# Kernel tuning notes

Measured on AMD Instinct MI355X. Metric: run time of the kernel, lower is better.

## Reference

```python
import jax, jax.numpy as jnp
import numpy as np

N, E, G, F, H, L, NH, HD = 40000, 640000, 256, 9, 128, 3, 4, 32
EPS = 1e-5

def _ln(x, g, b):
    m = jnp.mean(x, axis=-1, keepdims=True)
    v = jnp.mean((x - m) ** 2, axis=-1, keepdims=True)
    return (x - m) * jax.lax.rsqrt(v + EPS) * g + b

def _forward(floats, edge_index, batch):
    (x, pos, emb_w, emb_b, edge_w1, edge_b1, edge_w2, edge_b2,
     node_w1, node_b1, node_w2, node_b2, qkv_w, qkv_b, out_w, out_b,
     ln1_g, ln1_b, ln2_g, ln2_b, ff_w1, ff_b1, ff_w2, ff_b2,
     cls_w1, cls_b1, cls_w2, cls_b2) = floats
    src, dst = edge_index[0], edge_index[1]  # PyG: x_j = x[src], x_i = x[dst], aggregate at dst
    dist = jnp.linalg.norm(pos[dst] - pos[src], axis=-1, keepdims=True)  # [E,1]
    h = x @ emb_w + emb_b  # [N,H]
    for l in range(L):
        # message: edge_mlp(cat[x_i, x_j, dist])
        ef = jnp.concatenate([h[dst], h[src], dist], axis=-1)  # [E,2H+1]
        m = jax.nn.silu(ef @ edge_w1[l] + edge_b1[l])
        m = jax.nn.silu(m @ edge_w2[l] + edge_b2[l])  # [E,H]
        aggr = jax.ops.segment_sum(m, dst, num_segments=N)  # [N,H]
        u = jax.nn.silu(jnp.concatenate([h, aggr], axis=-1) @ node_w1[l] + node_b1[l])
        u = u @ node_w2[l] + node_b2[l]
        h = h + u  # residual in GAHT.forward
    # per-graph mean pooling (faithful to masked-mean loop)
    sums = jax.ops.segment_sum(h, batch, num_segments=G)  # [G,H]
    cnts = jax.ops.segment_sum(jnp.ones((N,), h.dtype), batch, num_segments=G)
    g = sums / jnp.maximum(cnts, 1.0)[:, None]  # [G,H]
    # 2-layer post-norm transformer encoder (batch=1, seq=G), relu FFN, eval mode (no dropout)
    scale = 1.0 / jnp.sqrt(jnp.asarray(HD, g.dtype))
    for t in range(2):
        qkv = g @ qkv_w[t] + qkv_b[t]  # [G,3H]
        q, k, v = jnp.split(qkv, 3, axis=-1)
        q = q.reshape(G, NH, HD); k = k.reshape(G, NH, HD); v = v.reshape(G, NH, HD)
        att = jax.nn.softmax(jnp.einsum('qhd,khd->hqk', q, k) * scale, axis=-1)
        o = jnp.einsum('hqk,khd->qhd', att, v).reshape(G, H)
        o = o @ out_w[t] + out_b[t]
        g = _ln(g + o, ln1_g[t], ln1_b[t])
        ff = jax.nn.relu(g @ ff_w1[t] + ff_b1[t]) @ ff_w2[t] + ff_b2[t]
        g = _ln(g + ff, ln2_g[t], ln2_b[t])
    out = jax.nn.relu(g @ cls_w1 + cls_b1) @ cls_w2 + cls_b2  # [G,1]
    return out.squeeze(-1)  # [G]


def setup_inputs() -> dict:
    key = jax.random.key(0)
    ks = jax.random.split(key, 16)
    def p(k, shape, scale=0.08):
        return jax.random.normal(k, shape, dtype=jnp.float32) * scale
    return {
        'x': jax.random.normal(ks[0], (N, F), dtype=jnp.float32),
        'pos': jax.random.normal(ks[1], (N, 3), dtype=jnp.float32),
        'emb_w': p(ks[2], (F, H)), 'emb_b': jnp.zeros((H,), jnp.float32),
        'edge_w1': p(ks[3], (L, 2 * H + 1, H)), 'edge_b1': jnp.zeros((L, H), jnp.float32),
        'edge_w2': p(ks[4], (L, H, H)), 'edge_b2': jnp.zeros((L, H), jnp.float32),
        'node_w1': p(ks[5], (L, 2 * H, H)), 'node_b1': jnp.zeros((L, H), jnp.float32),
        'node_w2': p(ks[6], (L, H, H)), 'node_b2': jnp.zeros((L, H), jnp.float32),
        'qkv_w': p(ks[7], (2, H, 3 * H)), 'qkv_b': jnp.zeros((2, 3 * H), jnp.float32),
        'out_w': p(ks[8], (2, H, H)), 'out_b': jnp.zeros((2, H), jnp.float32),
        'ln1_g': jnp.ones((2, H), jnp.float32), 'ln1_b': jnp.zeros((2, H), jnp.float32),
        'ln2_g': jnp.ones((2, H), jnp.float32), 'ln2_b': jnp.zeros((2, H), jnp.float32),
        'ff_w1': p(ks[9], (2, H, 2 * H)), 'ff_b1': jnp.zeros((2, 2 * H), jnp.float32),
        'ff_w2': p(ks[10], (2, 2 * H, H)), 'ff_b2': jnp.zeros((2, H), jnp.float32),
        'cls_w1': p(ks[11], (H, H // 2)), 'cls_b1': jnp.zeros((H // 2,), jnp.float32),
        'cls_w2': p(ks[12], (H // 2, 1)), 'cls_b2': jnp.zeros((1,), jnp.float32),
        'edge_index': jax.random.randint(ks[13], (2, E), 0, N),
        'batch': jnp.sort(jax.random.randint(ks[14], (N,), 0, G)),
    }


def reference(x, pos, emb_w, emb_b, edge_w1, edge_b1, edge_w2, edge_b2,
              node_w1, node_b1, node_w2, node_b2, qkv_w, qkv_b, out_w, out_b,
              ln1_g, ln1_b, ln2_g, ln2_b, ff_w1, ff_b1, ff_w2, ff_b2,
              cls_w1, cls_b1, cls_w2, cls_b2, edge_index, batch):
    floats = (x, pos, emb_w, emb_b, edge_w1, edge_b1, edge_w2, edge_b2,
              node_w1, node_b1, node_w2, node_b2, qkv_w, qkv_b, out_w, out_b,
              ln1_g, ln1_b, ln2_g, ln2_b, ff_w1, ff_b1, ff_w2, ff_b2,
              cls_w1, cls_b1, cls_w2, cls_b2)
    return _forward(floats, edge_index, batch)
```

## Files before the change

kernel.cpp:

```cpp
#include <hip/hip_runtime.h>
#include <hip/hip_bf16.h>
#include <stdint.h>

#define NN 40000
#define EE 640000
#define GG 256
#define FFE 9
#define HH 128

typedef __bf16 bf16;
typedef __bf16 bf16x8 __attribute__((ext_vector_type(8)));
typedef float f32x4 __attribute__((ext_vector_type(4)));

__device__ __forceinline__ f32x4 mfma16(bf16x8 a, bf16x8 b, f32x4 c){
  return __builtin_amdgcn_mfma_f32_16x16x32_bf16(a, b, c, 0, 0, 0);
}
__device__ __forceinline__ float silu_f(float x){
  return x * __builtin_amdgcn_rcpf(1.0f + __expf(-x));
}
__device__ __forceinline__ uint16_t bfb(float x){ bf16 h=(bf16)x; return *(uint16_t*)&h; }
__device__ __forceinline__ int swz(int row, int cb){
  return row*256 + (cb ^ ((row & 7) << 4));
}

__global__ __launch_bounds__(256) void k_prep(
    const float* __restrict__ edge_w1, const float* __restrict__ edge_w2,
    const float* __restrict__ node_w1, const float* __restrict__ node_w2,
    const float* __restrict__ edge_b1,
    const float* __restrict__ x, const float* __restrict__ emb_w,
    const float* __restrict__ emb_b,
    bf16* __restrict__ wcatT, bf16* __restrict__ w2T,
    bf16* __restrict__ nw1T, bf16* __restrict__ nw2T,
    float* __restrict__ bcat, float* __restrict__ h,
    int* __restrict__ cnt)
{
  int b = blockIdx.x, tid = threadIdx.x;
  if (b < 192){
    int l = b/64; int t2 = (b%64)*256 + tid;
    int n = t2 >> 7, k = t2 & 127;
    wcatT[(size_t)l*32768 + n*128 + k] = (bf16)edge_w1[(size_t)l*32896 + k*128 + n];
  } else if (b < 384){
    int lb = b - 192; int l = lb/64; int t2 = (lb%64)*256 + tid;
    int n = t2 >> 7, k = t2 & 127;
    wcatT[(size_t)l*32768 + 16384 + n*128 + k] = (bf16)edge_w1[(size_t)l*32896 + (128+k)*128 + n];
  } else if (b < 576){
    int lb = b - 384; int l = lb/64; int t2 = (lb%64)*256 + tid;
    int n = t2 >> 7, k = t2 & 127;
    w2T[(size_t)l*16384 + n*128 + k] = (bf16)edge_w2[(size_t)l*16384 + k*128 + n];
  } else if (b < 960){
    int lb = b - 576; int l = lb/128; int t2 = (lb%128)*256 + tid;
    int n = t2 >> 8, k = t2 & 255;
    nw1T[(size_t)l*32768 + n*256 + k] = (bf16)node_w1[(size_t)l*32768 + k*128 + n];
  } else if (b < 1152){
    int lb = b - 960; int l = lb/64; int t2 = (lb%64)*256 + tid;
    int n = t2 >> 7, k = t2 & 127;
    nw2T[(size_t)l*16384 + n*128 + k] = (bf16)node_w2[(size_t)l*16384 + k*128 + n];
  } else if (b < 1155){
    int l = b - 1152;
    bcat[l*256 + tid] = (tid < 128) ? edge_b1[l*128 + tid] : 0.0f;
  } else if (b < 1312){
    int i = (b - 1155)*256 + tid;
    if (i < NN) cnt[i] = 0;
  } else {
    int idx = (b - 1312)*256 + tid;
    int n = idx >> 7, f = idx & 127;
    float s = emb_b[f];
    const float* xr = x + n*FFE;
    #pragma unroll
    for (int k=0;k<FFE;++k) s += xr[k]*emb_w[k*HH + f];
    h[idx] = s;
  }
}

__global__ __launch_bounds__(256) void k_hist(const int* __restrict__ dst, int* __restrict__ cnt){
  int e = blockIdx.x*256 + threadIdx.x;
  if (e < EE) atomicAdd(&cnt[dst[e]], 1);
}

__global__ __launch_bounds__(1024) void k_scanA(const int* __restrict__ cnt,
    int* __restrict__ cursor, int* __restrict__ partials, int n)
{
  __shared__ int s_wsum[16];
  int tid = threadIdx.x, lane = tid & 63, wv = tid >> 6;
  int i = blockIdx.x*4096 + tid*4;
  int c0 = (i  <n)? cnt[i  ] : 0;
  int c1 = (i+1<n)? cnt[i+1] : 0;
  int c2 = (i+2<n)? cnt[i+2] : 0;
  int c3 = (i+3<n)? cnt[i+3] : 0;
  int t0 = c0, t1 = t0+c1, t2 = t1+c2, t3 = t2+c3;
  int xx = t3;
  #pragma unroll
  for (int off=1; off<64; off<<=1){ int t = __shfl_up(xx, off); if (lane>=off) xx += t; }
  if (lane==63) s_wsum[wv] = xx;
  __syncthreads();
  if (wv==0 && lane<16){
    int y = s_wsum[lane];
    #pragma unroll
    for (int off=1; off<16; off<<=1){ int t = __shfl_up(y, off, 16); if (lane>=off) y += t; }
    s_wsum[lane] = y;
  }
  __syncthreads();
  int woff = wv ? s_wsum[wv-1] : 0;
  int eb = woff + xx - t3;
  if (i  <n) cursor[i  ] = eb;
  if (i+1<n) cursor[i+1] = eb + t0;
  if (i+2<n) cursor[i+2] = eb + t1;
  if (i+3<n) cursor[i+3] = eb + t2;
  if (tid==1023) partials[blockIdx.x] = woff + xx;
}

__global__ __launch_bounds__(64) void k_scanB(int* __restrict__ partials, int nb){
  int lane = threadIdx.x;
  int v = (lane < nb) ? partials[lane] : 0;
  int x = v;
  #pragma unroll
  for (int off=1; off<64; off<<=1){ int t = __shfl_up(x, off); if (lane>=off) x += t; }
  if (lane < nb) partials[lane] = x - v;
}

__global__ __launch_bounds__(256) void k_scatter(
    const int* __restrict__ ei, const float* __restrict__ pos,
    int* __restrict__ cursor, const int* __restrict__ offs, int4* __restrict__ rec)
{
  int e = blockIdx.x*256 + threadIdx.x;
  if (e >= EE) return;
  int s = ei[e], d = ei[EE + e];
  int p = atomicAdd(&cursor[d], 1) + offs[d >> 12];
  float dx = pos[d*3+0]-pos[s*3+0];
  float dy = pos[d*3+1]-pos[s*3+1];
  float dz = pos[d*3+2]-pos[s*3+2];
  int4 rc; rc.x = s; rc.y = d; rc.z = __float_as_int(sqrtf(dx*dx+dy*dy+dz*dz)); rc.w = 0;
  rec[p] = rc;
}

__global__ __launch_bounds__(256) void k_pgen(
    const float* __restrict__ h, const bf16* __restrict__ wct,
    const float* __restrict__ bcv, bf16* __restrict__ P, float* __restrict__ aggr)
{
  __shared__ bf16 SA[64][136];
  __shared__ bf16 SW[128][136];
  int tid = threadIdx.x, lane = tid & 63, w = tid >> 6;
  int rsel = lane & 15, hi = lane >> 4;
  int m0 = blockIdx.x * 64;
  f32x4 z = {0.f,0.f,0.f,0.f};
  #pragma unroll
  for (int it=0; it<8; ++it)
    *(f32x4*)(aggr + (size_t)m0*128 + (size_t)(tid + it*256)*4) = z;
  #pragma unroll
  for (int it=0; it<4; ++it){
    int idx = tid + it*256;
    int row = idx >> 4, cg = (idx & 15)*8;
    const float* sp = h + (size_t)(m0+row)*128 + cg;
    f32x4 u0 = *(const f32x4*)sp, u1v = *(const f32x4*)(sp+4);
    bf16x8 vv;
    vv[0]=(bf16)u0[0]; vv[1]=(bf16)u0[1]; vv[2]=(bf16)u0[2]; vv[3]=(bf16)u0[3];
    vv[4]=(bf16)u1v[0]; vv[5]=(bf16)u1v[1]; vv[6]=(bf16)u1v[2]; vv[7]=(bf16)u1v[3];
    *(bf16x8*)&SA[row][cg] = vv;
  }
  __syncthreads();
  int urow = w*16 + rsel;
  for (int nh=0; nh<2; ++nh){
    #pragma unroll
    for (int it=0; it<8; ++it){
      int idx = tid + it*256;
      int row = idx >> 4, cg = (idx & 15)*8;
      *(bf16x8*)&SW[row][cg] = *(const bf16x8*)(wct + (size_t)(nh*128+row)*128 + cg);
    }
    __syncthreads();
    f32x4 acc[8];
    #pragma unroll
    for (int nt=0;nt<8;++nt)
      #pragma unroll
      for (int r=0;r<4;++r) acc[nt][r]=0.f;
    #pragma unroll
    for (int ks=0; ks<4; ++ks){
      int kb = ks*32 + hi*8;
      bf16x8 fa = *(const bf16x8*)&SA[urow][kb];
      #pragma unroll
      for (int nt=0;nt<8;++nt){
        bf16x8 fw = *(const bf16x8*)&SW[nt*16 + rsel][kb];
        acc[nt] = mfma16(fw, fa, acc[nt]);
      }
    }
    __syncthreads();
    #pragma unroll
    for (int nt=0;nt<8;++nt){
      int nb = nh*128 + nt*16 + 4*hi;
      f32x4 b4 = *(const f32x4*)(bcv + nb);
      uint2 pk;
      pk.x = (unsigned)bfb(acc[nt][0] + b4[0]) | ((unsigned)bfb(acc[nt][1] + b4[1]) << 16);
      pk.y = (unsigned)bfb(acc[nt][2] + b4[2]) | ((unsigned)bfb(acc[nt][3] + b4[3]) << 16);
      *(uint2*)(P + (size_t)(m0+urow)*256 + nb) = pk;
    }
  }
}

template<bool DOP>
__global__ __launch_bounds__(256) void k_node(
    float* h, float* aggr,
    const bf16* __restrict__ nw1t,
    const bf16* __restrict__ nw2t,
    const bf16* __restrict__ wct,
    const float* __restrict__ nb1, const float* __restrict__ nb2,
    const float* __restrict__ bcv,
    bf16* __restrict__ P)
{
  __shared__ bf16 SA[64][132];
  __shared__ bf16 SW[128][72];
  __shared__ bf16 SU[64][132];
  int tid = threadIdx.x, lane = tid & 63, w = tid >> 6;
  int rsel = lane & 15, hi = lane >> 4;
  int m0 = blockIdx.x * 64;
  int urow = w*16 + rsel;
  int grow = m0 + urow;

  f32x4 acc[8];
  #pragma unroll
  for (int nt=0;nt<8;++nt)
    #pragma unroll
    for (int r=0;r<4;++r) acc[nt][r]=0.f;

  for (int kq=0; kq<4; ++kq){
    const float* src = (kq < 2) ? (h + (size_t)m0*128 + kq*64)
                                : (aggr + (size_t)m0*128 + (kq-2)*64);
    #pragma unroll
    for (int it=0; it<2; ++it){
      int g = tid + it*256;
      int row = g >> 3, cg = (g & 7)*8;
      const float* sp = src + (size_t)row*128 + cg;
      f32x4 u0 = *(const f32x4*)sp, u1v = *(const f32x4*)(sp+4);
      bf16x8 vv;
      vv[0]=(bf16)u0[0]; vv[1]=(bf16)u0[1]; vv[2]=(bf16)u0[2]; vv[3]=(bf16)u0[3];
      vv[4]=(bf16)u1v[0]; vv[5]=(bf16)u1v[1]; vv[6]=(bf16)u1v[2]; vv[7]=(bf16)u1v[3];
      *(bf16x8*)&SA[row][cg] = vv;
    }
    #pragma unroll
    for (int it=0; it<4; ++it){
      int g = tid + it*256;
      int row = g >> 3, cg = (g & 7)*8;
      *(bf16x8*)&SW[row][cg] = *(const bf16x8*)(nw1t + (size_t)row*256 + kq*64 + cg);
    }
    __syncthreads();
    #pragma unroll
    for (int ks=0; ks<2; ++ks){
      int kb = ks*32 + hi*8;
      bf16x8 fa = *(const bf16x8*)&SA[w*16 + rsel][kb];
      #pragma unroll
      for (int nt=0;nt<8;++nt){
        bf16x8 fw = *(const bf16x8*)&SW[nt*16 + rsel][kb];
        acc[nt] = mfma16(fw, fa, acc[nt]);
      }
    }
    __syncthreads();
  }

  #pragma unroll
  for (int nt=0;nt<8;++nt){
    int nb = nt*16 + 4*hi;
    f32x4 b4 = *(const f32x4*)(nb1 + nb);
    uint2 pk;
    pk.x = (unsigned)bfb(silu_f(acc[nt][0] + b4[0])) | ((unsigned)bfb(silu_f(acc[nt][1] + b4[1])) << 16);
    pk.y = (unsigned)bfb(silu_f(acc[nt][2] + b4[2])) | ((unsigned)bfb(silu_f(acc[nt][3] + b4[3])) << 16);
    *(uint2*)&SU[urow][nb] = pk;
  }
  __syncthreads();

  #pragma unroll
  for (int nt=0;nt<8;++nt)
    #pragma unroll
    for (int r=0;r<4;++r) acc[nt][r]=0.f;
  for (int kq=0; kq<2; ++kq){
    #pragma unroll
    for (int it=0; it<4; ++it){
      int g = tid + it*256;
      int row = g >> 3, cg = (g & 7)*8;
      *(bf16x8*)&SW[row][cg] = *(const bf16x8*)(nw2t + (size_t)row*128 + kq*64 + cg);
    }
    __syncthreads();
    #pragma unroll
    for (int ks=0; ks<2; ++ks){
      int kb = ks*32 + hi*8;
      bf16x8 fa = *(const bf16x8*)&SU[w*16 + rsel][kq*64 + kb];
      #pragma unroll
      for (int nt=0;nt<8;++nt){
        bf16x8 fw = *(const bf16x8*)&SW[nt*16 + rsel][kb];
        acc[nt] = mfma16(fw, fa, acc[nt]);
      }
    }
    __syncthreads();
  }

  #pragma unroll
  for (int nt=0;nt<8;++nt){
    int nb = nt*16 + 4*hi;
    f32x4 b4 = *(const f32x4*)(nb2 + nb);
    f32x4 h4 = *(const f32x4*)(h + (size_t)grow*128 + nb);
    f32x4 v;
    #pragma unroll
    for (int r=0;r<4;++r) v[r] = h4[r] + acc[nt][r] + b4[r];
    *(f32x4*)(h + (size_t)grow*128 + nb) = v;
    uint2 pk;
    pk.x = (unsigned)bfb(v[0]) | ((unsigned)bfb(v[1]) << 16);
    pk.y = (unsigned)bfb(v[2]) | ((unsigned)bfb(v[3]) << 16);
    *(uint2*)&SA[urow][nb] = pk;
  }
  __syncthreads();

  if (DOP){
    for (int nh=0; nh<2; ++nh){
      #pragma unroll
      for (int nt=0;nt<8;++nt)
        #pragma unroll
        for (int r=0;r<4;++r) acc[nt][r]=0.f;
      for (int kq=0; kq<2; ++kq){
        #pragma unroll
        for (int it=0; it<4; ++it){
          int g = tid + it*256;
          int row = g >> 3, cg = (g & 7)*8;
          *(bf16x8*)&SW[row][cg] = *(const bf16x8*)(wct + (size_t)(nh*128+row)*128 + kq*64 + cg);
        }
        __syncthreads();
        #pragma unroll
        for (int ks=0; ks<2; ++ks){
          int kb = ks*32 + hi*8;
          bf16x8 fa = *(const bf16x8*)&SA[w*16 + rsel][kq*64 + kb];
          #pragma unroll
          for (int nt=0;nt<8;++nt){
            bf16x8 fw = *(const bf16x8*)&SW[nt*16 + rsel][kb];
            acc[nt] = mfma16(fw, fa, acc[nt]);
          }
        }
        __syncthreads();
      }
      #pragma unroll
      for (int nt=0;nt<8;++nt){
        int nb = nh*128 + nt*16 + 4*hi;
        f32x4 b4 = *(const f32x4*)(bcv + nb);
        uint2 pk;
        pk.x = (unsigned)bfb(acc[nt][0] + b4[0]) | ((unsigned)bfb(acc[nt][1] + b4[1]) << 16);
        pk.y = (unsigned)bfb(acc[nt][2] + b4[2]) | ((unsigned)bfb(acc[nt][3] + b4[3]) << 16);
        *(uint2*)(P + (size_t)grow*256 + nb) = pk;
      }
    }
    f32x4 z = {0.f,0.f,0.f,0.f};
    #pragma unroll
    for (int it=0; it<8; ++it){
      int idx = tid + it*256;
      *(f32x4*)(aggr + (size_t)m0*128 + (size_t)idx*4) = z;
    }
  }
}

__global__ __launch_bounds__(512, 6) void k_edge(
    const bf16* __restrict__ P, const bf16* __restrict__ w2t,
    const float* __restrict__ w1r, const float* __restrict__ b2,
    const int4* __restrict__ rec, float* __restrict__ aggr)
{
  __shared__ char smem[32768];
  __shared__ int s_dst[128];
  __shared__ int s_segid[128];
  __shared__ int s_segdst[128];
  __shared__ bf16 s_sel[16][136];
  __shared__ int s_misc[4];
  int tid = threadIdx.x, lane = tid & 63, w = tid >> 6;
  int rsel = lane & 15, hi = lane >> 4;
  int bid = blockIdx.x;
  int swb = (bid & 7) * (EE/128/8) + (bid >> 3);
  int e0 = swb * 128;
  int col = w*16 + rsel;

  bf16x8 fb[4];
  #pragma unroll
  for (int ks=0;ks<4;++ks)
    fb[ks] = *(const bf16x8*)(w2t + (size_t)col*128 + ks*32 + hi*8);

  if (tid == 0){
    s_misc[0] = (e0 == 0) ? -2147483647 : rec[e0-1].y;
    s_misc[1] = (e0 + 128 >= EE) ? -2147483647 : rec[e0+128].y;
  }

  int cq = (tid & 15)*8;
  int er = tid >> 4;
  int4 rc[4];
  #pragma unroll
  for (int it=0; it<4; ++it) rc[it] = rec[e0 + er + it*32];
  uint4 pau[4], pbu[4];
  #pragma unroll
  for (int it=0; it<4; ++it){
    pau[it] = *(const uint4*)(P + ((size_t)rc[it].y << 8) + cq);
    pbu[it] = *(const uint4*)(P + ((size_t)rc[it].x << 8) + 128 + cq);
  }
  if (cq == 0){
    #pragma unroll
    for (int it=0; it<4; ++it) s_dst[er + it*32] = rc[it].y;
  }
  f32x4 wr0 = *(const f32x4*)(w1r + cq);
  f32x4 wr1 = *(const f32x4*)(w1r + cq + 4);
  #pragma unroll
  for (int it=0; it<4; ++it){
    float dist = __int_as_float(rc[it].z);
    bf16x8 mm;
    #pragma unroll
    for (int j=0;j<4;++j){
      unsigned ua = ((const unsigned*)&pau[it])[j];
      unsigned ub = ((const unsigned*)&pbu[it])[j];
      float al = __uint_as_float(ua << 16);
      float ah = __uint_as_float(ua & 0xFFFF0000u);
      float bl = __uint_as_float(ub << 16);
      float bh = __uint_as_float(ub & 0xFFFF0000u);
      float wlo = (j<2) ? wr0[2*j]   : wr1[2*(j-2)];
      float whi = (j<2) ? wr0[2*j+1] : wr1[2*(j-2)+1];
      mm[2*j]   = (bf16)silu_f(al + bl + dist*wlo);
      mm[2*j+1] = (bf16)silu_f(ah + bh + dist*whi);
    }
    *(bf16x8*)(smem + swz(er + it*32, cq*2)) = mm;
  }
  __syncthreads();

  if (w == 0){
    int d0 = s_dst[2*lane], d1 = s_dst[2*lane+1];
    int dm1 = (lane == 0) ? 0 : s_dst[2*lane-1];
    int h0 = (lane == 0) ? 1 : (d0 != dm1);
    int h1 = (d1 != d0);
    int p = h0 + h1, x = p;
    #pragma unroll
    for (int off=1; off<64; off<<=1){ int t = __shfl_up(x, off); if (lane>=off) x += t; }
    int excl = x - p;
    int id0 = excl + h0 - 1;
    int id1 = excl + p - 1;
    s_segid[2*lane]   = id0;
    s_segid[2*lane+1] = id1;
    if (h0) s_segdst[id0] = d0;
    if (h1) s_segdst[id1] = d1;
    if (lane == 63) s_misc[2] = id1 + 1;
  }

  f32x4 acc[8];
  #pragma unroll
  for (int mt=0;mt<8;++mt)
    #pragma unroll
    for (int r=0;r<4;++r) acc[mt][r]=0.f;
  #pragma unroll
  for (int mt=0;mt<8;++mt){
    #pragma unroll
    for (int ks=0;ks<4;++ks){
      bf16x8 fa = *(const bf16x8*)(smem + swz(mt*16 + rsel, ks*64 + hi*16));
      acc[mt] = mfma16(fa, fb[ks], acc[mt]);
    }
  }
  __syncthreads();

  float bb = b2[col];
  #pragma unroll
  for (int mt=0;mt<8;++mt){
    uint2 pk;
    pk.x = (unsigned)bfb(silu_f(acc[mt][0] + bb)) | ((unsigned)bfb(silu_f(acc[mt][1] + bb)) << 16);
    pk.y = (unsigned)bfb(silu_f(acc[mt][2] + bb)) | ((unsigned)bfb(silu_f(acc[mt][3] + bb)) << 16);
    *(uint2*)(smem + col*256 + ((mt*32 + hi*8) ^ ((col & 7) << 4))) = pk;
  }
  __syncthreads();

  bf16x8 gb[4];
  #pragma unroll
  for (int ks=0;ks<4;++ks)
    gb[ks] = *(const bf16x8*)(smem + col*256 + ((ks*64 + hi*16) ^ ((col & 7) << 4)));
  int nseg = s_misc[2];
  bool openL = (s_dst[0]   == s_misc[0]);
  bool openR = (s_dst[127] == s_misc[1]);
  const bf16 ONE = (bf16)1.0f, ZERO = (bf16)0.0f;
  for (int st = 0; st < nseg; st += 16){
    __syncthreads();
    #pragma unroll
    for (int k4=0;k4<4;++k4){
      int idx = tid + k4*512;
      int s = idx >> 7, e = idx & 127;
      s_sel[s][e] = (s_segid[e] == st + s) ? ONE : ZERO;
    }
    __syncthreads();
    f32x4 racc = {0.f,0.f,0.f,0.f};
    #pragma unroll
    for (int ks=0;ks<4;++ks){
      bf16x8 sa = *(const bf16x8*)&s_sel[rsel][ks*32 + hi*8];
      racc = mfma16(sa, gb[ks], racc);
    }
    #pragma unroll
    for (int r=0;r<4;++r){
      int s = st + 4*hi + r;
      if (s < nseg){
        float v = racc[r];
        size_t off = (size_t)s_segdst[s]*128 + col;
        bool atom = (s == 0 && openL) || (s == nseg-1 && openR);
        if (atom) atomicAdd(&aggr[off], v);
        else      aggr[off] = v;
      }
    }
  }
}

__device__ __forceinline__ int lbound(const int* a, int n, int key){
  int lo=0, hi=n;
  while (lo<hi){ int mid=(lo+hi)>>1; if (a[mid]<key) lo=mid+1; else hi=mid; }
  return lo;
}

__global__ __launch_bounds__(384) void k_pool_qkv(
    const float* __restrict__ h, const int* __restrict__ batch,
    const float* __restrict__ wq, const float* __restrict__ bq,
    float* __restrict__ gbuf, float* __restrict__ qkvb)
{
  __shared__ float sg[128];
  int gr = blockIdx.x, tid = threadIdx.x;
  if (tid < 128){
    int lo = lbound(batch, NN, gr), hi2 = lbound(batch, NN, gr+1);
    float s = 0.f;
    for (int n=lo;n<hi2;++n) s += h[(size_t)n*HH + tid];
    int c = hi2 - lo; if (c < 1) c = 1;
    s /= (float)c;
    sg[tid] = s; gbuf[gr*128 + tid] = s;
  }
  __syncthreads();
  float a = bq[tid];
  for (int k=0;k<128;++k) a += sg[k]*wq[k*384 + tid];
  qkvb[gr*384 + tid] = a;
}

template<int MODE>
__global__ __launch_bounds__(128) void k_tail(
    const float* __restrict__ qkv, const float* __restrict__ wo,
    const float* __restrict__ bo, const float* __restrict__ l1g,
    const float* __restrict__ l1b, const float* __restrict__ w1,
    const float* __restrict__ b1f, const float* __restrict__ w2,
    const float* __restrict__ b2f, const float* __restrict__ l2g,
    const float* __restrict__ l2b, float* __restrict__ gbuf,
    const float* __restrict__ wq2, const float* __restrict__ bq2,
    float* __restrict__ qkvb2,
    const float* __restrict__ cw1, const float* __restrict__ cb1,
    const float* __restrict__ cw2, const float* __restrict__ cb2,
    float* __restrict__ out)
{
  __shared__ float sq[128];
  __shared__ float ss[4][256];
  __shared__ float so[128];
  __shared__ float st[256];
  __shared__ float red[4];
  int r = blockIdx.x, tid = threadIdx.x;
  sq[tid] = qkv[r*384 + tid];
  __syncthreads();
  const float scale = 0.17677669529663687f;
  for (int i=tid; i<1024; i+=128){
    int hh = i >> 8, j = i & 255;
    const float* kr = qkv + j*384 + 128 + hh*32;
    const float* qr = sq + hh*32;
    float s=0;
    #pragma unroll
    for (int d=0;d<32;++d) s += qr[d]*kr[d];
    ss[hh][j] = s*scale;
  }
  __syncthreads();
  int hh = tid >> 5, sl = tid & 31;
  float m = -1e30f;
  #pragma unroll
  for (int q8=0;q8<8;++q8) m = fmaxf(m, ss[hh][sl + q8*32]);
  #pragma unroll
  for (int off=16; off; off>>=1) m = fmaxf(m, __shfl_xor(m, off, 32));
  float sum = 0.f;
  #pragma unroll
  for (int q8=0;q8<8;++q8){
    float e = __expf(ss[hh][sl+q8*32] - m);
    ss[hh][sl+q8*32] = e;
    sum += e;
  }
  #pragma unroll
  for (int off=16; off; off>>=1) sum += __shfl_xor(sum, off, 32);
  float inv = __builtin_amdgcn_rcpf(sum);
  __syncthreads();
  float accv = 0.f;
  for (int j=0;j<256;++j) accv += ss[hh][j]*qkv[j*384 + 256 + hh*32 + sl];
  so[tid] = accv*inv;
  __syncthreads();
  float a = bo[tid];
  for (int k=0;k<128;++k) a += so[k]*wo[k*128 + tid];
  float val = gbuf[r*128 + tid] + a;
  {
    float s = val, q = val*val;
    #pragma unroll
    for (int off=32; off; off>>=1){ s += __shfl_xor(s, off); q += __shfl_xor(q, off); }
    int lane = tid & 63, wv = tid >> 6;
    if (lane==0){ red[wv*2]=s; red[wv*2+1]=q; }
    __syncthreads();
    float S = red[0]+red[2], Q = red[1]+red[3];
    float mean = S*(1.0f/128.0f);
    float var = Q*(1.0f/128.0f) - mean*mean;
    float ninv = rsqrtf(var + 1e-5f);
    val = (val-mean)*ninv*l1g[tid] + l1b[tid];
  }
  sq[tid] = val;
  __syncthreads();
  float a0 = b1f[tid], a1 = b1f[tid+128];
  for (int k=0;k<128;++k){
    float gv = sq[k];
    a0 += gv*w1[k*256 + tid];
    a1 += gv*w1[k*256 + tid + 128];
  }
  st[tid]     = fmaxf(a0, 0.f);
  st[tid+128] = fmaxf(a1, 0.f);
  __syncthreads();
  float b = b2f[tid];
  for (int k=0;k<256;++k) b += st[k]*w2[k*128 + tid];
  float val2 = val + b;
  {
    float s = val2, q = val2*val2;
    #pragma unroll
    for (int off=32; off; off>>=1){ s += __shfl_xor(s, off); q += __shfl_xor(q, off); }
    int lane = tid & 63, wv = tid >> 6;
    __syncthreads();
    if (lane==0){ red[wv*2]=s; red[wv*2+1]=q; }
    __syncthreads();
    float S = red[0]+red[2], Q = red[1]+red[3];
    float mean = S*(1.0f/128.0f);
    float var = Q*(1.0f/128.0f) - mean*mean;
    float ninv = rsqrtf(var + 1e-5f);
    val2 = (val2-mean)*ninv*l2g[tid] + l2b[tid];
  }
  gbuf[r*128 + tid] = val2;
  if (MODE == 0){
    sq[tid] = val2;
    __syncthreads();
    float q0 = bq2[tid], q1 = bq2[tid+128], q2 = bq2[tid+256];
    for (int k=0;k<128;++k){
      float gv = sq[k];
      const float* wr = wq2 + k*384;
      q0 += gv*wr[tid]; q1 += gv*wr[tid+128]; q2 += gv*wr[tid+256];
    }
    qkvb2[r*384+tid]=q0; qkvb2[r*384+tid+128]=q1; qkvb2[r*384+tid+256]=q2;
  }
  if (MODE == 1){
    so[tid] = val2;
    __syncthreads();
    if (tid < 64){
      float c = cb1[tid];
      for (int k=0;k<128;++k) c += so[k]*cw1[k*64 + tid];
      c = fmaxf(c, 0.f);
      float p = c * cw2[tid];
      #pragma unroll
      for (int off=32; off; off>>=1) p += __shfl_xor(p, off);
      if (tid==0) out[r] = p + cb2[0];
    }
  }
}

extern "C" void kernel_launch(void* const* d_in, const int* in_sizes, int n_in,
                              void* d_out, int out_size, void* d_ws, size_t ws_size,
                              hipStream_t stream)
{
  (void)in_sizes; (void)n_in; (void)out_size; (void)ws_size;
  const float* x      = (const float*)d_in[0];
  const float* pos    = (const float*)d_in[1];
  const float* emb_w  = (const float*)d_in[2];
  const float* emb_b  = (const float*)d_in[3];
  const float* edge_w1= (const float*)d_in[4];
  const float* edge_b1= (const float*)d_in[5];
  const float* edge_w2= (const float*)d_in[6];
  const float* edge_b2= (const float*)d_in[7];
  const float* node_w1= (const float*)d_in[8];
  const float* node_b1= (const float*)d_in[9];
  const float* node_w2= (const float*)d_in[10];
  const float* node_b2= (const float*)d_in[11];
  const float* qkv_w  = (const float*)d_in[12];
  const float* qkv_b  = (const float*)d_in[13];
  const float* out_w  = (const float*)d_in[14];
  const float* out_b  = (const float*)d_in[15];
  const float* ln1_g  = (const float*)d_in[16];
  const float* ln1_b  = (const float*)d_in[17];
  const float* ln2_g  = (const float*)d_in[18];
  const float* ln2_b  = (const float*)d_in[19];
  const float* ff_w1  = (const float*)d_in[20];
  const float* ff_b1  = (const float*)d_in[21];
  const float* ff_w2  = (const float*)d_in[22];
  const float* ff_b2  = (const float*)d_in[23];
  const float* cls_w1 = (const float*)d_in[24];
  const float* cls_b1 = (const float*)d_in[25];
  const float* cls_w2 = (const float*)d_in[26];
  const float* cls_b2 = (const float*)d_in[27];
  const int* ei       = (const int*)d_in[28];
  const int* batch    = (const int*)d_in[29];
  float* out = (float*)d_out;

  uint8_t* wp = (uint8_t*)d_ws;
  auto take = [&](size_t nb)->void*{ void* r = wp; wp += (nb + 255) & ~(size_t)255; return r; };
  float* h      = (float*)take((size_t)NN*HH*4);
  bf16*  P      = (bf16*) take((size_t)NN*256*2);
  float* aggr   = (float*)take((size_t)NN*HH*4);
  int*   cnt    = (int*)  take((size_t)NN*4);
  int*   cursor = (int*)  take((size_t)NN*4);
  int*   parts  = (int*)  take((size_t)64*4);
  int4*  rec    = (int4*) take((size_t)EE*16);
  bf16*  wcatT  = (bf16*) take((size_t)3*256*128*2);
  bf16*  w2T    = (bf16*) take((size_t)3*128*128*2);
  bf16*  nw1T   = (bf16*) take((size_t)3*128*256*2);
  bf16*  nw2T   = (bf16*) take((size_t)3*128*128*2);
  float* bcat   = (float*)take((size_t)3*256*4);
  float* gbuf   = (float*)take((size_t)GG*HH*4);
  float* qkvb   = (float*)take((size_t)GG*384*4);
  float* qkvb2  = (float*)take((size_t)GG*384*4);

  dim3 b256(256);
  k_prep<<<dim3(21312), b256, 0, stream>>>(edge_w1, edge_w2, node_w1, node_w2,
    edge_b1, x, emb_w, emb_b, wcatT, w2T, nw1T, nw2T, bcat, h, cnt);
  k_hist<<<dim3(EE/256), b256, 0, stream>>>(ei + EE, cnt);
  k_scanA<<<dim3(10), dim3(1024), 0, stream>>>(cnt, cursor, parts, NN);
  k_scanB<<<dim3(1), dim3(64), 0, stream>>>(parts, 10);
  k_scatter<<<dim3(EE/256), b256, 0, stream>>>(ei, pos, cursor, parts, rec);

  k_pgen<<<dim3(625), b256, 0, stream>>>(h, wcatT, bcat, P, aggr);

  for (int l=0;l<3;++l){
    k_edge<<<dim3(EE/128), dim3(512), 0, stream>>>(P, w2T + (size_t)l*16384,
      edge_w1 + ((size_t)l*257 + 256)*128, edge_b2 + (size_t)l*128, rec, aggr);
    if (l < 2){
      k_node<true><<<dim3(625), b256, 0, stream>>>(h, aggr,
        nw1T + (size_t)l*32768, nw2T + (size_t)l*16384, wcatT + (size_t)(l+1)*32768,
        node_b1 + (size_t)l*128, node_b2 + (size_t)l*128, bcat + (size_t)(l+1)*256, P);
    } else {
      k_node<false><<<dim3(625), b256, 0, stream>>>(h, aggr,
        nw1T + (size_t)l*32768, nw2T + (size_t)l*16384, wcatT,
        node_b1 + (size_t)l*128, node_b2 + (size_t)l*128, bcat, P);
    }
  }

  k_pool_qkv<<<dim3(GG), dim3(384), 0, stream>>>(h, batch, qkv_w, qkv_b, gbuf, qkvb);
  k_tail<0><<<dim3(GG), dim3(128), 0, stream>>>(qkvb, out_w, out_b,
    ln1_g, ln1_b, ff_w1, ff_b1, ff_w2, ff_b2, ln2_g, ln2_b, gbuf,
    qkv_w + (size_t)128*384, qkv_b + 384, qkvb2,
    nullptr, nullptr, nullptr, nullptr, nullptr);
  k_tail<1><<<dim3(GG), dim3(128), 0, stream>>>(qkvb2, out_w + (size_t)128*128, out_b + 128,
    ln1_g + 128, ln1_b + 128, ff_w1 + (size_t)128*256, ff_b1 + 256,
    ff_w2 + (size_t)256*128, ff_b2 + 128, ln2_g + 128, ln2_b + 128, gbuf,
    nullptr, nullptr, nullptr,
    cls_w1, cls_b1, cls_w2, cls_b2, out);
}
```

Measured before the change: 631.3 us.

## Widen node kernel to 512 threads, tile embedding in LDS, fold scanB into scatter

The node-update kernel now runs 8 waves per 64-row block, with each wave owning 16 output columns across all rows instead of 16 rows across all columns. It also adds a separate LDS buffer for the updated h so the next-layer projection no longer reuses SA. The embedding part of k_prep now stages x, emb_w and emb_b in shared memory per 64-node tile, which cuts its block count from 21312 to 1937. The single-block partial scan is folded into each k_scatter block, removing one launch at the cost of redundant tiny scans. More LDS per node block may reduce occupancy.

```diff
diff --git a/kernel.cpp b/kernel.cpp
--- a/kernel.cpp
+++ b/kernel.cpp
@@ -34,6 +34,9 @@
     float* __restrict__ bcat, float* __restrict__ h,
     int* __restrict__ cnt)
 {
+  __shared__ float sx[64][9];
+  __shared__ float swt[9][128];
+  __shared__ float sbv[128];
   int b = blockIdx.x, tid = threadIdx.x;
   if (b < 192){
     int l = b/64; int t2 = (b%64)*256 + tid;
@@ -62,13 +65,26 @@
     int i = (b - 1155)*256 + tid;
     if (i < NN) cnt[i] = 0;
   } else {
-    int idx = (b - 1312)*256 + tid;
-    int n = idx >> 7, f = idx & 127;
-    float s = emb_b[f];
-    const float* xr = x + n*FFE;
-    #pragma unroll
-    for (int k=0;k<FFE;++k) s += xr[k]*emb_w[k*HH + f];
-    h[idx] = s;
+    int m0 = (b - 1312) * 64;
+    if (tid < 128) sbv[tid] = emb_b[tid];
+    for (int i = tid; i < 1152; i += 256) swt[i>>7][i&127] = emb_w[i];
+    for (int i = tid; i < 576; i += 256) sx[i/9][i%9] = x[(size_t)m0*9 + i];
+    __syncthreads();
+    int row = tid >> 2, c0 = (tid & 3) * 32;
+    float xr[9];
+    #pragma unroll
+    for (int k=0;k<9;++k) xr[k] = sx[row][k];
+    for (int j=0;j<32;j+=4){
+      f32x4 a;
+      #pragma unroll
+      for (int r=0;r<4;++r) a[r] = sbv[c0+j+r];
+      #pragma unroll
+      for (int k=0;k<9;++k){
+        #pragma unroll
+        for (int r=0;r<4;++r) a[r] += xr[k]*swt[k][c0+j+r];
+      }
+      *(f32x4*)(h + (size_t)(m0+row)*128 + c0 + j) = a;
+    }
   }
 }
 
@@ -109,23 +125,24 @@
   if (tid==1023) partials[blockIdx.x] = woff + xx;
 }
 
-__global__ __launch_bounds__(64) void k_scanB(int* __restrict__ partials, int nb){
-  int lane = threadIdx.x;
-  int v = (lane < nb) ? partials[lane] : 0;
-  int x = v;
-  #pragma unroll
-  for (int off=1; off<64; off<<=1){ int t = __shfl_up(x, off); if (lane>=off) x += t; }
-  if (lane < nb) partials[lane] = x - v;
-}
-
 __global__ __launch_bounds__(256) void k_scatter(
     const int* __restrict__ ei, const float* __restrict__ pos,
-    int* __restrict__ cursor, const int* __restrict__ offs, int4* __restrict__ rec)
-{
-  int e = blockIdx.x*256 + threadIdx.x;
+    int* __restrict__ cursor, const int* __restrict__ parts, int4* __restrict__ rec)
+{
+  __shared__ int offs_s[16];
+  int tid = threadIdx.x;
+  if (tid < 16){
+    int v = (tid < 10) ? parts[tid] : 0;
+    int xp = v;
+    #pragma unroll
+    for (int off=1; off<16; off<<=1){ int t = __shfl_up(xp, off, 16); if (tid>=off) xp += t; }
+    offs_s[tid] = xp - v;
+  }
+  __syncthreads();
+  int e = blockIdx.x*256 + tid;
   if (e >= EE) return;
   int s = ei[e], d = ei[EE + e];
-  int p = atomicAdd(&cursor[d], 1) + offs[d >> 12];
+  int p = atomicAdd(&cursor[d], 1) + offs_s[d >> 12];
   float dx = pos[d*3+0]-pos[s*3+0];
   float dy = pos[d*3+1]-pos[s*3+1];
   float dz = pos[d*3+2]-pos[s*3+2];
@@ -196,7 +213,7 @@
 }
 
 template<bool DOP>
-__global__ __launch_bounds__(256) void k_node(
+__global__ __launch_bounds__(512) void k_node(
     float* h, float* aggr,
     const bf16* __restrict__ nw1t,
     const bf16* __restrict__ nw2t,
@@ -205,28 +222,26 @@
     const float* __restrict__ bcv,
     bf16* __restrict__ P)
 {
-  __shared__ bf16 SA[64][132];
+  __shared__ bf16 SA[64][68];
   __shared__ bf16 SW[128][72];
   __shared__ bf16 SU[64][132];
+  __shared__ bf16 SH[64][132];
   int tid = threadIdx.x, lane = tid & 63, w = tid >> 6;
   int rsel = lane & 15, hi = lane >> 4;
   int m0 = blockIdx.x * 64;
-  int urow = w*16 + rsel;
-  int grow = m0 + urow;
-
-  f32x4 acc[8];
-  #pragma unroll
-  for (int nt=0;nt<8;++nt)
-    #pragma unroll
-    for (int r=0;r<4;++r) acc[nt][r]=0.f;
+  int nbase = w*16 + 4*hi;
+
+  f32x4 acc[4];
+  #pragma unroll
+  for (int rt=0;rt<4;++rt)
+    #pragma unroll
+    for (int r=0;r<4;++r) acc[rt][r]=0.f;
 
   for (int kq=0; kq<4; ++kq){
     const float* src = (kq < 2) ? (h + (size_t)m0*128 + kq*64)
                                 : (aggr + (size_t)m0*128 + (kq-2)*64);
-    #pragma unroll
-    for (int it=0; it<2; ++it){
-      int g = tid + it*256;
-      int row = g >> 3, cg = (g & 7)*8;
+    {
+      int g = tid, row = g >> 3, cg = (g & 7)*8;
       const float* sp = src + (size_t)row*128 + cg;
       f32x4 u0 = *(const f32x4*)sp, u1v = *(const f32x4*)(sp+4);
       bf16x8 vv;
@@ -235,119 +250,116 @@
       *(bf16x8*)&SA[row][cg] = vv;
     }
     #pragma unroll
-    for (int it=0; it<4; ++it){
-      int g = tid + it*256;
-      int row = g >> 3, cg = (g & 7)*8;
+    for (int it=0; it<2; ++it){
+      int g = tid + it*512, row = g >> 3, cg = (g & 7)*8;
       *(bf16x8*)&SW[row][cg] = *(const bf16x8*)(nw1t + (size_t)row*256 + kq*64 + cg);
     }
     __syncthreads();
     #pragma unroll
     for (int ks=0; ks<2; ++ks){
       int kb = ks*32 + hi*8;
-      bf16x8 fa = *(const bf16x8*)&SA[w*16 + rsel][kb];
-      #pragma unroll
-      for (int nt=0;nt<8;++nt){
-        bf16x8 fw = *(const bf16x8*)&SW[nt*16 + rsel][kb];
-        acc[nt] = mfma16(fw, fa, acc[nt]);
+      bf16x8 fw = *(const bf16x8*)&SW[w*16 + rsel][kb];
+      #pragma unroll
+      for (int rt=0; rt<4; ++rt){
+        bf16x8 fa = *(const bf16x8*)&SA[rt*16 + rsel][kb];
+        acc[rt] = mfma16(fw, fa, acc[rt]);
       }
     }
     __syncthreads();
   }
 
-  #pragma unroll
-  for (int nt=0;nt<8;++nt){
-    int nb = nt*16 + 4*hi;
-    f32x4 b4 = *(const f32x4*)(nb1 + nb);
-    uint2 pk;
-    pk.x = (unsigned)bfb(silu_f(acc[nt][0] + b4[0])) | ((unsigned)bfb(silu_f(acc[nt][1] + b4[1])) << 16);
-    pk.y = (unsigned)bfb(silu_f(acc[nt][2] + b4[2])) | ((unsigned)bfb(silu_f(acc[nt][3] + b4[3])) << 16);
-    *(uint2*)&SU[urow][nb] = pk;
-  }
-  __syncthreads();
-
-  #pragma unroll
-  for (int nt=0;nt<8;++nt)
-    #pragma unroll
-    for (int r=0;r<4;++r) acc[nt][r]=0.f;
+  {
+    f32x4 b4 = *(const f32x4*)(nb1 + nbase);
+    #pragma unroll
+    for (int rt=0; rt<4; ++rt){
+      uint2 pk;
+      pk.x = (unsigned)bfb(silu_f(acc[rt][0]+b4[0])) | ((unsigned)bfb(silu_f(acc[rt][1]+b4[1]))<<16);
+      pk.y = (unsigned)bfb(silu_f(acc[rt][2]+b4[2])) | ((unsigned)bfb(silu_f(acc[rt][3]+b4[3]))<<16);
+      *(uint2*)&SU[rt*16 + rsel][nbase] = pk;
+    }
+  }
+
+  #pragma unroll
+  for (int rt=0;rt<4;++rt)
+    #pragma unroll
+    for (int r=0;r<4;++r) acc[rt][r]=0.f;
   for (int kq=0; kq<2; ++kq){
     #pragma unroll
-    for (int it=0; it<4; ++it){
-      int g = tid + it*256;
-      int row = g >> 3, cg = (g & 7)*8;
+    for (int it=0; it<2; ++it){
+      int g = tid + it*512, row = g >> 3, cg = (g & 7)*8;
       *(bf16x8*)&SW[row][cg] = *(const bf16x8*)(nw2t + (size_t)row*128 + kq*64 + cg);
     }
     __syncthreads();
     #pragma unroll
     for (int ks=0; ks<2; ++ks){
       int kb = ks*32 + hi*8;
-      bf16x8 fa = *(const bf16x8*)&SU[w*16 + rsel][kq*64 + kb];
-      #pragma unroll
-      for (int nt=0;nt<8;++nt){
-        bf16x8 fw = *(const bf16x8*)&SW[nt*16 + rsel][kb];
-        acc[nt] = mfma16(fw, fa, acc[nt]);
+      bf16x8 fw = *(const bf16x8*)&SW[w*16 + rsel][kb];
+      #pragma unroll
+      for (int rt=0; rt<4; ++rt){
+        bf16x8 fa = *(const bf16x8*)&SU[rt*16 + rsel][kq*64 + kb];
+        acc[rt] = mfma16(fw, fa, acc[rt]);
       }
     }
     __syncthreads();
   }
 
-  #pragma unroll
-  for (int nt=0;nt<8;++nt){
-    int nb = nt*16 + 4*hi;
-    f32x4 b4 = *(const f32x4*)(nb2 + nb);
-    f32x4 h4 = *(const f32x4*)(h + (size_t)grow*128 + nb);
-    f32x4 v;
-    #pragma unroll
-    for (int r=0;r<4;++r) v[r] = h4[r] + acc[nt][r] + b4[r];
-    *(f32x4*)(h + (size_t)grow*128 + nb) = v;
-    uint2 pk;
-    pk.x = (unsigned)bfb(v[0]) | ((unsigned)bfb(v[1]) << 16);
-    pk.y = (unsigned)bfb(v[2]) | ((unsigned)bfb(v[3]) << 16);
-    *(uint2*)&SA[urow][nb] = pk;
-  }
-  __syncthreads();
+  {
+    f32x4 c4 = *(const f32x4*)(nb2 + nbase);
+    #pragma unroll
+    for (int rt=0; rt<4; ++rt){
+      int grow = m0 + rt*16 + rsel;
+      f32x4 h4 = *(const f32x4*)(h + (size_t)grow*128 + nbase);
+      f32x4 v;
+      #pragma unroll
+      for (int r=0;r<4;++r) v[r] = h4[r] + acc[rt][r] + c4[r];
+      *(f32x4*)(h + (size_t)grow*128 + nbase) = v;
+      uint2 pk;
+      pk.x = (unsigned)bfb(v[0]) | ((unsigned)bfb(v[1]) << 16);
+      pk.y = (unsigned)bfb(v[2]) | ((unsigned)bfb(v[3]) << 16);
+      *(uint2*)&SH[rt*16 + rsel][nbase] = pk;
+    }
+  }
 
   if (DOP){
     for (int nh=0; nh<2; ++nh){
-      #pragma unroll
-      for (int nt=0;nt<8;++nt)
+      f32x4 a3[4];
+      #pragma unroll
+      for (int rt=0;rt<4;++rt)
         #pragma unroll
-        for (int r=0;r<4;++r) acc[nt][r]=0.f;
+        for (int r=0;r<4;++r) a3[rt][r]=0.f;
       for (int kq=0; kq<2; ++kq){
         #pragma unroll
-        for (int it=0; it<4; ++it){
-          int g = tid + it*256;
-          int row = g >> 3, cg = (g & 7)*8;
+        for (int it=0; it<2; ++it){
+          int g = tid + it*512, row = g >> 3, cg = (g & 7)*8;
           *(bf16x8*)&SW[row][cg] = *(const bf16x8*)(wct + (size_t)(nh*128+row)*128 + kq*64 + cg);
         }
         __syncthreads();
         #pragma unroll
         for (int ks=0; ks<2; ++ks){
           int kb = ks*32 + hi*8;
-          bf16x8 fa = *(const bf16x8*)&SA[w*16 + rsel][kq*64 + kb];
+          bf16x8 fw = *(const bf16x8*)&SW[w*16 + rsel][kb];
           #pragma unroll
-          for (int nt=0;nt<8;++nt){
-            bf16x8 fw = *(const bf16x8*)&SW[nt*16 + rsel][kb];
-            acc[nt] = mfma16(fw, fa, acc[nt]);
+          for (int rt=0; rt<4; ++rt){
+            bf16x8 fa = *(const bf16x8*)&SH[rt*16 + rsel][kq*64 + kb];
+            a3[rt] = mfma16(fw, fa, a3[rt]);
           }
         }
         __syncthreads();
       }
-      #pragma unroll
-      for (int nt=0;nt<8;++nt){
-        int nb = nh*128 + nt*16 + 4*hi;
-        f32x4 b4 = *(const f32x4*)(bcv + nb);
+      f32x4 bb4 = *(const f32x4*)(bcv + nh*128 + nbase);
+      #pragma unroll
+      for (int rt=0; rt<4; ++rt){
+        int grow = m0 + rt*16 + rsel;
         uint2 pk;
-        pk.x = (unsigned)bfb(acc[nt][0] + b4[0]) | ((unsigned)bfb(acc[nt][1] + b4[1]) << 16);
-        pk.y = (unsigned)bfb(acc[nt][2] + b4[2]) | ((unsigned)bfb(acc[nt][3] + b4[3]) << 16);
-        *(uint2*)(P + (size_t)grow*256 + nb) = pk;
+        pk.x = (unsigned)bfb(a3[rt][0]+bb4[0]) | ((unsigned)bfb(a3[rt][1]+bb4[1])<<16);
+        pk.y = (unsigned)bfb(a3[rt][2]+bb4[2]) | ((unsigned)bfb(a3[rt][3]+bb4[3])<<16);
+        *(uint2*)(P + (size_t)grow*256 + nh*128 + nbase) = pk;
       }
     }
     f32x4 z = {0.f,0.f,0.f,0.f};
     #pragma unroll
-    for (int it=0; it<8; ++it){
-      int idx = tid + it*256;
-      *(f32x4*)(aggr + (size_t)m0*128 + (size_t)idx*4) = z;
-    }
+    for (int it=0; it<4; ++it)
+      *(f32x4*)(aggr + (size_t)m0*128 + (size_t)(tid + it*512)*4) = z;
   }
 }
 
@@ -705,11 +717,10 @@
   float* qkvb2  = (float*)take((size_t)GG*384*4);
 
   dim3 b256(256);
-  k_prep<<<dim3(21312), b256, 0, stream>>>(edge_w1, edge_w2, node_w1, node_w2,
+  k_prep<<<dim3(1937), b256, 0, stream>>>(edge_w1, edge_w2, node_w1, node_w2,
     edge_b1, x, emb_w, emb_b, wcatT, w2T, nw1T, nw2T, bcat, h, cnt);
   k_hist<<<dim3(EE/256), b256, 0, stream>>>(ei + EE, cnt);
   k_scanA<<<dim3(10), dim3(1024), 0, stream>>>(cnt, cursor, parts, NN);
-  k_scanB<<<dim3(1), dim3(64), 0, stream>>>(parts, 10);
   k_scatter<<<dim3(EE/256), b256, 0, stream>>>(ei, pos, cursor, parts, rec);
 
   k_pgen<<<dim3(625), b256, 0, stream>>>(h, wcatT, bcat, P, aggr);
@@ -718,11 +729,11 @@
     k_edge<<<dim3(EE/128), dim3(512), 0, stream>>>(P, w2T + (size_t)l*16384,
       edge_w1 + ((size_t)l*257 + 256)*128, edge_b2 + (size_t)l*128, rec, aggr);
     if (l < 2){
-      k_node<true><<<dim3(625), b256, 0, stream>>>(h, aggr,
+      k_node<true><<<dim3(625), dim3(512), 0, stream>>>(h, aggr,
         nw1T + (size_t)l*32768, nw2T + (size_t)l*16384, wcatT + (size_t)(l+1)*32768,
         node_b1 + (size_t)l*128, node_b2 + (size_t)l*128, bcat + (size_t)(l+1)*256, P);
     } else {
-      k_node<false><<<dim3(625), b256, 0, stream>>>(h, aggr,
+      k_node<false><<<dim3(625), dim3(512), 0, stream>>>(h, aggr,
         nw1T + (size_t)l*32768, nw2T + (size_t)l*16384, wcatT,
         node_b1 + (size_t)l*128, node_b2 + (size_t)l*128, bcat, P);
     }
```

New measurement: 629.1 us. Within noise of the previous version (-0.3%).
